# Optimization experiments

Hardware: AMD Instinct MI355X
Metric: run time of the kernel (lower is better)

## Reference

```python
import jax, jax.numpy as jnp
import numpy as np

SPARSITY = 0.01  # sparsity_threshold (softshrink lambda)


def _cas(n):
    # Hartley cas kernel: cos + sin
    t = jnp.arange(n, dtype=jnp.float32)
    a = 2.0 * jnp.pi * jnp.outer(t, t) / n
    return jnp.cos(a) + jnp.sin(a)


def _dht2d(x):
    # Faithful to source 4-D branch: transforms the LAST TWO axes (W and C)
    B, H, W, C = x.shape
    y = jnp.einsum('bhwc,cd->bhwd', x, _cas(C))          # contract channel axis
    return jnp.einsum('vw,bhwd->bhvd', _cas(W), y)       # contract width axis


def setup_inputs() -> dict:
    key = jax.random.key(0)
    k0, k1, k2, k3, k4 = jax.random.split(key, 5)
    B, H, W, C = 1, 180, 360, 512
    nb, bs, f = 8, 64, 1  # num_blocks, block_size, hidden_size_factor
    scale = 0.02
    x = jax.random.normal(k0, (B, H, W, C), jnp.float32)
    w1 = scale * jax.random.normal(k1, (2, nb, bs, bs * f), jnp.float32)
    b1 = scale * jax.random.normal(k2, (2, nb, bs * f), jnp.float32)
    w2 = scale * jax.random.normal(k3, (2, nb, bs * f, bs), jnp.float32)
    b2 = scale * jax.random.normal(k4, (2, nb, bs), jnp.float32)
    return {"x": x, "w1": w1, "b1": b1, "w2": w2, "b2": b2}


def reference(x, w1, b1, w2, b2):
    bias = x
    B, H, W, C = x.shape
    nb, bs = w1.shape[1], w1.shape[2]

    xh = _dht2d(x).reshape(B, H, W, nb, bs)                       # X_H_k
    xn = jnp.roll(jnp.flip(xh, axis=(1, 2)), shift=(1, 1), axis=(1, 2))  # X_H_{-k}

    # layer 1: 0.5*(Xk(w0+w1) + Xn(w0-w1)) + b  (algebraic regroup of the 4 einsums)
    w1a, w1b = w1[0] + w1[1], w1[0] - w1[1]
    o1k = jax.nn.relu(0.5 * (jnp.einsum('bhwki,kio->bhwko', xh, w1a)
                             + jnp.einsum('bhwki,kio->bhwko', xn, w1b)) + b1[0])
    o1n = jax.nn.relu(0.5 * (jnp.einsum('bhwki,kio->bhwko', xn, w1a)
                             + jnp.einsum('bhwki,kio->bhwko', xh, w1b)) + b1[1])

    # layer 2 (faithfully reproduces source bug: o2n consumes o2k, bias included)
    w2a, w2b = w2[0] + w2[1], w2[0] - w2[1]
    o2k = 0.5 * (jnp.einsum('bhwki,kio->bhwko', o1k, w2a)
                 + jnp.einsum('bhwki,kio->bhwko', o1n, w2b)) + b2[0]
    o2n = 0.5 * (jnp.einsum('bhwki,kio->bhwko', o1n, w2a)
                 + jnp.einsum('bhwki,kio->bhwko', o2k, w2b)) + b2[1]

    y = (o2k + o2n).reshape(B, H, W, C)
    y = jnp.sign(y) * jax.nn.relu(jnp.abs(y) - SPARSITY)          # softshrink
    y = _dht2d(y) / (W * C)                                       # idht2d normalization
    return y + bias
```

## Files before the change

kernel.cpp:

```cpp
#include <hip/hip_runtime.h>
#include <math.h>

#define HH 180
#define WDIM 360
#define CDIM 512
#define NP 64800
#define PL 184320

typedef unsigned short u16;
typedef __attribute__((ext_vector_type(8))) short short8;
typedef __attribute__((ext_vector_type(4))) float f4;

__device__ __forceinline__ u16 f2bf(float f){
    unsigned u = __float_as_uint(f);
    return (u16)((u + 0x7fffu + ((u >> 16) & 1u)) >> 16);
}
__device__ __forceinline__ void gl_lds16(const void* g, void* l){
    __builtin_amdgcn_global_load_lds((const __attribute__((address_space(1))) void*)g,
                                     (__attribute__((address_space(3))) void*)l, 16, 0, 0);
}

__global__ void prep(const float* __restrict__ w1, const float* __restrict__ w2,
                     u16* __restrict__ casC, u16* __restrict__ casW, u16* __restrict__ wts)
{
    int idx = blockIdx.x * 256 + threadIdx.x;
    if (idx < 512*512){
        int i = idx >> 9, j = idx & 511;
        int m = (i * j) & 511;
        float a = (float)m * (6.283185307179586f / 512.0f);
        float s, c; __sincosf(a, &s, &c);
        casC[idx] = f2bf(c + s);
    }
    if (idx < 360*384){
        int i = idx / 384, j = idx - (idx / 384) * 384;
        u16 v = 0;
        if (j < 360){
            int m = (i * j) % 360;
            float a = (float)m * (6.283185307179586f / 360.0f);
            float s, c; __sincosf(a, &s, &c);
            v = f2bf(c + s);
        }
        casW[idx] = v;
    }
    if (idx < 131072){
        int s = idx >> 15, r = idx & 32767;
        int kb = r >> 12, o = (r >> 6) & 63, ii = r & 63;
        const float* w = (s < 2) ? w1 : w2;
        float v0 = w[kb*4096 + ii*64 + o];
        float v1 = w[32768 + kb*4096 + ii*64 + o];
        float v = 0.5f * ((s & 1) ? (v0 - v1) : (v0 + v1));
        wts[idx] = f2bf(v);
    }
}

template<int ASTAGE, int STORE, int SWAP>
__global__ __launch_bounds__(256)
void gemm_k(const void* __restrict__ A, int ldA, long long sA, int clampA,
            const u16* __restrict__ B, int ldB, long long sB,
            void* __restrict__ C, long long sC, int Mreal,
            const float* __restrict__ X, float scale, int nK, int nbx)
{
    __shared__ u16 As[2][4096];
    __shared__ u16 Bs[2][4096];

    const int tid = threadIdx.x, wv = tid >> 6, l = tid & 63;
    const int l16 = l & 15, quad = l >> 4;
    const int z = blockIdx.z;

    int bx, by;
    if constexpr (SWAP){
        int n = gridDim.x;
        int q = n >> 3, r = n & 7;
        int xcd = blockIdx.x & 7, idx = blockIdx.x >> 3;
        int swz = (xcd < r ? xcd*(q+1) : r*(q+1) + (xcd-r)*q) + idx;
        bx = swz / nbx;
        by = swz - bx * nbx;
    } else {
        bx = blockIdx.x;
        by = blockIdx.y;
    }
    const int row0 = bx * 128, col0 = by * 128;

    const int rh = wv & 1, c0 = wv >> 1;

    const u16* gB = B + sB * z + (long long)(col0 + rh*64 + l) * ldB;

    const u16* gA = nullptr;
    const float* gAf = nullptr; int arow = 0, cb = 0;
    if constexpr (ASTAGE == 0){
        int r = row0 + rh*64 + l; r = r <= clampA ? r : clampA;
        gA = (const u16*)A + sA * z + (long long)r * ldA;
    } else {
        int r = row0 + (tid >> 1); r = r <= clampA ? r : clampA;
        gAf  = (const float*)A + (long long)r * ldA + (tid & 1) * 16;
        arow = tid >> 1;
        cb   = (tid & 1) * 2;
    }

    f4 acc[4][4];
    #pragma unroll
    for (int mt = 0; mt < 4; ++mt)
        #pragma unroll
        for (int nt = 0; nt < 4; ++nt)
            acc[mt][nt] = (f4)0.0f;

    const int mrow = (wv >> 1) * 64, ncol = (wv & 1) * 64;

    float4 f0, f1, f2, f3;

    auto stageB = [&](int buf, int k0){
        gl_lds16(gB + k0 + c0*8,     &Bs[buf][c0*1024     + rh*512]);
        gl_lds16(gB + k0 + (c0+2)*8, &Bs[buf][(c0+2)*1024 + rh*512]);
    };
    auto stageA = [&](int buf, int k0){
        gl_lds16(gA + k0 + c0*8,     &As[buf][c0*1024     + rh*512]);
        gl_lds16(gA + k0 + (c0+2)*8, &As[buf][(c0+2)*1024 + rh*512]);
    };
    auto issueA = [&](int k0){
        const float* p = gAf + k0;
        f0 = *(const float4*)(p);
        f1 = *(const float4*)(p + 4);
        f2 = *(const float4*)(p + 8);
        f3 = *(const float4*)(p + 12);
    };
    auto writeA = [&](int buf){
        uint4 w0, w1;
        w0.x = (unsigned)f2bf(f0.x) | ((unsigned)f2bf(f0.y) << 16);
        w0.y = (unsigned)f2bf(f0.z) | ((unsigned)f2bf(f0.w) << 16);
        w0.z = (unsigned)f2bf(f1.x) | ((unsigned)f2bf(f1.y) << 16);
        w0.w = (unsigned)f2bf(f1.z) | ((unsigned)f2bf(f1.w) << 16);
        w1.x = (unsigned)f2bf(f2.x) | ((unsigned)f2bf(f2.y) << 16);
        w1.y = (unsigned)f2bf(f2.z) | ((unsigned)f2bf(f2.w) << 16);
        w1.z = (unsigned)f2bf(f3.x) | ((unsigned)f2bf(f3.y) << 16);
        w1.w = (unsigned)f2bf(f3.z) | ((unsigned)f2bf(f3.w) << 16);
        *(uint4*)&As[buf][cb*1024     + arow*8] = w0;
        *(uint4*)&As[buf][(cb+1)*1024 + arow*8] = w1;
    };

    stageB(0, 0);
    if constexpr (ASTAGE == 0){
        stageA(0, 0);
    } else {
        issueA(0);
        writeA(0);
    }
    __syncthreads();

    int cur = 0;
    for (int kt = 0; kt < nK; ++kt){
        const bool more = (kt + 1 < nK);
        const int k0n = (kt + 1) * 32;
        if (more){
            stageB(cur ^ 1, k0n);
            if constexpr (ASTAGE == 0) stageA(cur ^ 1, k0n);
            else                       issueA(k0n);
        }
        short8 af[4];
        #pragma unroll
        for (int mt = 0; mt < 4; ++mt)
            af[mt] = *(const short8*)&As[cur][quad*1024 + (mrow + mt*16 + l16)*8];
        #pragma unroll
        for (int nt = 0; nt < 4; ++nt){
            short8 bfv = *(const short8*)&Bs[cur][quad*1024 + (ncol + nt*16 + l16)*8];
            #pragma unroll
            for (int mt = 0; mt < 4; ++mt)
                acc[mt][nt] = __builtin_amdgcn_mfma_f32_16x16x32_bf16(af[mt], bfv, acc[mt][nt], 0, 0, 0);
        }
        if constexpr (ASTAGE == 1){
            if (more) writeA(cur ^ 1);
        }
        __syncthreads();
        cur ^= 1;
    }

    #pragma unroll
    for (int mt = 0; mt < 4; ++mt){
        #pragma unroll
        for (int i = 0; i < 4; ++i){
            int gr = row0 + mrow + mt*16 + quad*4 + i;
            if (gr >= Mreal) continue;
            int th = 0, tw = 0;
            if constexpr (STORE == 1){ th = gr / 360; tw = gr - th * 360; }
            #pragma unroll
            for (int nt = 0; nt < 4; ++nt){
                int gc = col0 + ncol + nt*16 + l16;
                if constexpr (STORE == 0){
                    ((u16*)C)[sC*z + (long long)gr*512 + gc] = f2bf(acc[mt][nt][i]);
                } else if constexpr (STORE == 1){
                    ((u16*)C)[((long long)th*512 + gc)*360 + tw] = f2bf(acc[mt][nt][i]);
                } else {
                    long long off = sC*z + (long long)gr*512 + gc;
                    ((float*)C)[off] = fmaf(acc[mt][nt][i], scale, X[off]);
                }
            }
        }
    }
}

__global__ __launch_bounds__(256)
void mlp_k(const u16* __restrict__ xh, const u16* __restrict__ wts,
           const float* __restrict__ b1, const float* __restrict__ b2,
           u16* __restrict__ yout)
{
    __shared__ u16 sW0[64*72], sW1[64*72];
    __shared__ u16 sXh[64*72], sXn[64*72], s1k[64*72], s1n[64*72];
    __shared__ float sb[256];

    const int tid = threadIdx.x;
    const int wv = tid >> 6, l = tid & 63, lane16 = l & 15, quad = l >> 4;
    const int kb = blockIdx.y;
    const int p0 = blockIdx.x * 64;
    const int w16 = wv * 16;

    if (tid < 64){
        sb[tid]       = b1[kb*64 + tid];
        sb[64 + tid]  = b1[512 + kb*64 + tid];
        sb[128 + tid] = b2[kb*64 + tid];
        sb[192 + tid] = b2[512 + kb*64 + tid];
    }
    {
        const int r = tid >> 2, sg = (tid & 3) * 16;
        const u16* s0 = wts + kb*4096 + r*64 + sg;
        const u16* s1 = wts + 32768 + kb*4096 + r*64 + sg;
        *(uint4*)&sW0[r*72 + sg]     = *(const uint4*)s0;
        *(uint4*)&sW0[r*72 + sg + 8] = *(const uint4*)(s0 + 8);
        *(uint4*)&sW1[r*72 + sg]     = *(const uint4*)s1;
        *(uint4*)&sW1[r*72 + sg + 8] = *(const uint4*)(s1 + 8);

        int p = p0 + r; int pc = p <= 64799 ? p : 64799;
        int h = pc / 360; int v = pc - h * 360;
        int hn = (h == 0) ? 0 : (180 - h);
        int vn = (v == 0) ? 0 : (360 - v);
        long long bh = (long long)pc * 512 + kb*64 + sg;
        long long bn = (long long)(hn*360 + vn) * 512 + kb*64 + sg;
        *(uint4*)&sXh[r*72 + sg]     = *(const uint4*)&xh[bh];
        *(uint4*)&sXh[r*72 + sg + 8] = *(const uint4*)&xh[bh + 8];
        *(uint4*)&sXn[r*72 + sg]     = *(const uint4*)&xh[bn];
        *(uint4*)&sXn[r*72 + sg + 8] = *(const uint4*)&xh[bn + 8];
    }
    __syncthreads();

    f4 aK[4], aN[4];
    #pragma unroll
    for (int nt = 0; nt < 4; ++nt){ aK[nt] = (f4)0.0f; aN[nt] = (f4)0.0f; }
    #pragma unroll
    for (int kq = 0; kq < 2; ++kq){
        short8 fxh = *(const short8*)&sXh[(w16 + lane16)*72 + kq*32 + quad*8];
        short8 fxn = *(const short8*)&sXn[(w16 + lane16)*72 + kq*32 + quad*8];
        #pragma unroll
        for (int nt = 0; nt < 4; ++nt){
            short8 wa = *(const short8*)&sW0[(nt*16 + lane16)*72 + kq*32 + quad*8];
            short8 wb = *(const short8*)&sW1[(nt*16 + lane16)*72 + kq*32 + quad*8];
            aK[nt] = __builtin_amdgcn_mfma_f32_16x16x32_bf16(fxh, wa, aK[nt], 0,0,0);
            aK[nt] = __builtin_amdgcn_mfma_f32_16x16x32_bf16(fxn, wb, aK[nt], 0,0,0);
            aN[nt] = __builtin_amdgcn_mfma_f32_16x16x32_bf16(fxn, wa, aN[nt], 0,0,0);
            aN[nt] = __builtin_amdgcn_mfma_f32_16x16x32_bf16(fxh, wb, aN[nt], 0,0,0);
        }
    }
    #pragma unroll
    for (int nt = 0; nt < 4; ++nt){
        int cc = nt*16 + lane16;
        #pragma unroll
        for (int i = 0; i < 4; ++i){
            int rr = w16 + quad*4 + i;
            float vk = fmaxf(aK[nt][i] + sb[cc], 0.f);
            float vn = fmaxf(aN[nt][i] + sb[64 + cc], 0.f);
            s1k[rr*72 + cc] = f2bf(vk);
            s1n[rr*72 + cc] = f2bf(vn);
        }
    }
    __syncthreads();

    {
        const int r = tid >> 2, sg = (tid & 3) * 16;
        const u16* s0 = wts + 65536 + kb*4096 + r*64 + sg;
        const u16* s1 = wts + 98304 + kb*4096 + r*64 + sg;
        *(uint4*)&sW0[r*72 + sg]     = *(const uint4*)s0;
        *(uint4*)&sW0[r*72 + sg + 8] = *(const uint4*)(s0 + 8);
        *(uint4*)&sW1[r*72 + sg]     = *(const uint4*)s1;
        *(uint4*)&sW1[r*72 + sg + 8] = *(const uint4*)(s1 + 8);
    }
    __syncthreads();

    f4 k2[4];
    #pragma unroll
    for (int nt = 0; nt < 4; ++nt) k2[nt] = (f4)0.0f;
    #pragma unroll
    for (int kq = 0; kq < 2; ++kq){
        short8 a1k = *(const short8*)&s1k[(w16 + lane16)*72 + kq*32 + quad*8];
        short8 a1n = *(const short8*)&s1n[(w16 + lane16)*72 + kq*32 + quad*8];
        #pragma unroll
        for (int nt = 0; nt < 4; ++nt){
            short8 wa = *(const short8*)&sW0[(nt*16 + lane16)*72 + kq*32 + quad*8];
            short8 wb = *(const short8*)&sW1[(nt*16 + lane16)*72 + kq*32 + quad*8];
            k2[nt] = __builtin_amdgcn_mfma_f32_16x16x32_bf16(a1k, wa, k2[nt], 0,0,0);
            k2[nt] = __builtin_amdgcn_mfma_f32_16x16x32_bf16(a1n, wb, k2[nt], 0,0,0);
        }
    }
    #pragma unroll
    for (int nt = 0; nt < 4; ++nt){
        int cc = nt*16 + lane16;
        #pragma unroll
        for (int i = 0; i < 4; ++i){
            int rr = w16 + quad*4 + i;
            float v2 = k2[nt][i] + sb[128 + cc];
            k2[nt][i] = v2;
            sXh[rr*72 + cc] = f2bf(v2);
        }
    }
    __syncthreads();

    f4 n2[4];
    #pragma unroll
    for (int nt = 0; nt < 4; ++nt) n2[nt] = (f4)0.0f;
    #pragma unroll
    for (int kq = 0; kq < 2; ++kq){
        short8 a1n = *(const short8*)&s1n[(w16 + lane16)*72 + kq*32 + quad*8];
        short8 a2k = *(const short8*)&sXh[(w16 + lane16)*72 + kq*32 + quad*8];
        #pragma unroll
        for (int nt = 0; nt < 4; ++nt){
            short8 wa = *(const short8*)&sW0[(nt*16 + lane16)*72 + kq*32 + quad*8];
            short8 wb = *(const short8*)&sW1[(nt*16 + lane16)*72 + kq*32 + quad*8];
            n2[nt] = __builtin_amdgcn_mfma_f32_16x16x32_bf16(a1n, wa, n2[nt], 0,0,0);
            n2[nt] = __builtin_amdgcn_mfma_f32_16x16x32_bf16(a2k, wb, n2[nt], 0,0,0);
        }
    }
    #pragma unroll
    for (int nt = 0; nt < 4; ++nt){
        int cc = nt*16 + lane16;
        #pragma unroll
        for (int i = 0; i < 4; ++i){
            int rr = w16 + quad*4 + i;
            int p = p0 + rr;
            float y = k2[nt][i] + n2[nt][i] + sb[192 + cc];
            float ay = fabsf(y) - 0.01f;
            float r0 = ay > 0.f ? (y > 0.f ? ay : -ay) : 0.f;
            if (p < 64800) yout[(long long)p * 512 + kb*64 + cc] = f2bf(r0);
        }
    }
}

extern "C" void kernel_launch(void* const* d_in, const int* in_sizes, int n_in,
                              void* d_out, int out_size, void* d_ws, size_t ws_size,
                              hipStream_t stream) {
    const float* x  = (const float*)d_in[0];
    const float* w1 = (const float*)d_in[1];
    const float* b1 = (const float*)d_in[2];
    const float* w2 = (const float*)d_in[3];
    const float* b2 = (const float*)d_in[4];
    float* out = (float*)d_out;

    u16* ws   = (u16*)d_ws;
    u16* casC = ws;
    u16* casW = casC + 262144;
    u16* wts  = casW + 138240;
    u16* bufT = wts  + 131072;
    u16* bufP = bufT + 33177664;

    prep<<<1024, 256, 0, stream>>>(w1, w2, casC, casW, wts);

    dim3 gBig(2028, 1, 1);
    dim3 gW(3, 4, 180);
    dim3 gM(1013, 8, 1);

    gemm_k<1,1,1><<<gBig, 256, 0, stream>>>(x, 512, 0, 64799,
                                            casC, 512, 0,
                                            bufT, 0, 64800, nullptr, 0.f, 16, 4);
    gemm_k<0,0,0><<<gW, 256, 0, stream>>>(casW, 384, 0, 359,
                                          bufT, 360, (long long)PL,
                                          bufP, (long long)PL, 360, nullptr, 0.f, 12, 1);
    mlp_k<<<gM, 256, 0, stream>>>(bufP, wts, b1, b2, bufT);
    gemm_k<0,1,1><<<gBig, 256, 0, stream>>>(bufT, 512, 0, 64799,
                                            casC, 512, 0,
                                            bufP, 0, 64800, nullptr, 0.f, 16, 4);
    gemm_k<0,2,0><<<gW, 256, 0, stream>>>(casW, 384, 0, 359,
                                          bufP, 360, (long long)PL,
                                          out, (long long)PL, 360,
                                          x, 1.0f/184320.0f, 12, 1);
}
```

Measured before the change: 706.8 us.

## Pre-convert input to bf16 and use triple-buffered async LDS pipeline in GEMM

Adds a separate conversion kernel that turns the fp32 input into bf16, so every GEMM can stage A through direct global-to-LDS loads instead of register loads plus conversion. The GEMM main loop moves from double buffering to a three-stage ring: prefetch runs three tiles ahead, with explicit vmcnt waits and raw barriers in place of __syncthreads. This aims to hide global latency better and remove conversion work from the inner loop. The cost is an extra kernel pass over the input, 50% more LDS per block, and redundant clamped reloads of the last tile near the end of the loop.

```diff
diff --git a/kernel.cpp b/kernel.cpp
--- a/kernel.cpp
+++ b/kernel.cpp
@@ -53,15 +53,29 @@
     }
 }
 
-template<int ASTAGE, int STORE, int SWAP>
 __global__ __launch_bounds__(256)
-void gemm_k(const void* __restrict__ A, int ldA, long long sA, int clampA,
+void cvt_k(const float* __restrict__ x, u16* __restrict__ xb)
+{
+    long long i = ((long long)blockIdx.x * 256 + threadIdx.x) * 8;
+    float4 a = *(const float4*)(x + i);
+    float4 b = *(const float4*)(x + i + 4);
+    uint4 w;
+    w.x = (unsigned)f2bf(a.x) | ((unsigned)f2bf(a.y) << 16);
+    w.y = (unsigned)f2bf(a.z) | ((unsigned)f2bf(a.w) << 16);
+    w.z = (unsigned)f2bf(b.x) | ((unsigned)f2bf(b.y) << 16);
+    w.w = (unsigned)f2bf(b.z) | ((unsigned)f2bf(b.w) << 16);
+    *(uint4*)(xb + i) = w;
+}
+
+template<int STORE, int SWAP>
+__global__ __launch_bounds__(256)
+void gemm_k(const u16* __restrict__ A, int ldA, long long sA, int clampA,
             const u16* __restrict__ B, int ldB, long long sB,
             void* __restrict__ C, long long sC, int Mreal,
             const float* __restrict__ X, float scale, int nK, int nbx)
 {
-    __shared__ u16 As[2][4096];
-    __shared__ u16 Bs[2][4096];
+    __shared__ u16 As[3][4096];
+    __shared__ u16 Bs[3][4096];
 
     const int tid = threadIdx.x, wv = tid >> 6, l = tid & 63;
     const int l16 = l & 15, quad = l >> 4;
@@ -84,18 +98,8 @@
     const int rh = wv & 1, c0 = wv >> 1;
 
     const u16* gB = B + sB * z + (long long)(col0 + rh*64 + l) * ldB;
-
-    const u16* gA = nullptr;
-    const float* gAf = nullptr; int arow = 0, cb = 0;
-    if constexpr (ASTAGE == 0){
-        int r = row0 + rh*64 + l; r = r <= clampA ? r : clampA;
-        gA = (const u16*)A + sA * z + (long long)r * ldA;
-    } else {
-        int r = row0 + (tid >> 1); r = r <= clampA ? r : clampA;
-        gAf  = (const float*)A + (long long)r * ldA + (tid & 1) * 16;
-        arow = tid >> 1;
-        cb   = (tid & 1) * 2;
-    }
+    int ar = row0 + rh*64 + l; ar = ar <= clampA ? ar : clampA;
+    const u16* gA = A + sA * z + (long long)ar * ldA;
 
     f4 acc[4][4];
     #pragma unroll
@@ -106,55 +110,22 @@
 
     const int mrow = (wv >> 1) * 64, ncol = (wv & 1) * 64;
 
-    float4 f0, f1, f2, f3;
-
-    auto stageB = [&](int buf, int k0){
-        gl_lds16(gB + k0 + c0*8,     &Bs[buf][c0*1024     + rh*512]);
-        gl_lds16(gB + k0 + (c0+2)*8, &Bs[buf][(c0+2)*1024 + rh*512]);
-    };
-    auto stageA = [&](int buf, int k0){
-        gl_lds16(gA + k0 + c0*8,     &As[buf][c0*1024     + rh*512]);
-        gl_lds16(gA + k0 + (c0+2)*8, &As[buf][(c0+2)*1024 + rh*512]);
-    };
-    auto issueA = [&](int k0){
-        const float* p = gAf + k0;
-        f0 = *(const float4*)(p);
-        f1 = *(const float4*)(p + 4);
-        f2 = *(const float4*)(p + 8);
-        f3 = *(const float4*)(p + 12);
-    };
-    auto writeA = [&](int buf){
-        uint4 w0, w1;
-        w0.x = (unsigned)f2bf(f0.x) | ((unsigned)f2bf(f0.y) << 16);
-        w0.y = (unsigned)f2bf(f0.z) | ((unsigned)f2bf(f0.w) << 16);
-        w0.z = (unsigned)f2bf(f1.x) | ((unsigned)f2bf(f1.y) << 16);
-        w0.w = (unsigned)f2bf(f1.z) | ((unsigned)f2bf(f1.w) << 16);
-        w1.x = (unsigned)f2bf(f2.x) | ((unsigned)f2bf(f2.y) << 16);
-        w1.y = (unsigned)f2bf(f2.z) | ((unsigned)f2bf(f2.w) << 16);
-        w1.z = (unsigned)f2bf(f3.x) | ((unsigned)f2bf(f3.y) << 16);
-        w1.w = (unsigned)f2bf(f3.z) | ((unsigned)f2bf(f3.w) << 16);
-        *(uint4*)&As[buf][cb*1024     + arow*8] = w0;
-        *(uint4*)&As[buf][(cb+1)*1024 + arow*8] = w1;
-    };
-
-    stageB(0, 0);
-    if constexpr (ASTAGE == 0){
-        stageA(0, 0);
-    } else {
-        issueA(0);
-        writeA(0);
-    }
-    __syncthreads();
+    #define STAGE(buf, kt) do{ const int k0_ = (kt)*32;                          \
+        gl_lds16(gB + k0_ + c0*8,     &Bs[buf][c0*1024     + rh*512]);           \
+        gl_lds16(gB + k0_ + (c0+2)*8, &Bs[buf][(c0+2)*1024 + rh*512]);           \
+        gl_lds16(gA + k0_ + c0*8,     &As[buf][c0*1024     + rh*512]);           \
+        gl_lds16(gA + k0_ + (c0+2)*8, &As[buf][(c0+2)*1024 + rh*512]); }while(0)
+
+    STAGE(0, 0);
+    STAGE(1, 1);
+    STAGE(2, 2);
 
     int cur = 0;
     for (int kt = 0; kt < nK; ++kt){
-        const bool more = (kt + 1 < nK);
-        const int k0n = (kt + 1) * 32;
-        if (more){
-            stageB(cur ^ 1, k0n);
-            if constexpr (ASTAGE == 0) stageA(cur ^ 1, k0n);
-            else                       issueA(k0n);
-        }
+        asm volatile("s_waitcnt vmcnt(8)" ::: "memory");
+        __builtin_amdgcn_s_barrier();
+        __builtin_amdgcn_sched_barrier(0);
+
         short8 af[4];
         #pragma unroll
         for (int mt = 0; mt < 4; ++mt)
@@ -166,12 +137,16 @@
             for (int mt = 0; mt < 4; ++mt)
                 acc[mt][nt] = __builtin_amdgcn_mfma_f32_16x16x32_bf16(af[mt], bfv, acc[mt][nt], 0, 0, 0);
         }
-        if constexpr (ASTAGE == 1){
-            if (more) writeA(cur ^ 1);
-        }
-        __syncthreads();
-        cur ^= 1;
-    }
+
+        __builtin_amdgcn_sched_barrier(0);
+        __builtin_amdgcn_s_barrier();
+        __builtin_amdgcn_sched_barrier(0);
+
+        int nxt = kt + 3; if (nxt > nK - 1) nxt = nK - 1;
+        STAGE(cur, nxt);
+        cur = (cur == 2) ? 0 : cur + 1;
+    }
+    #undef STAGE
 
     #pragma unroll
     for (int mt = 0; mt < 4; ++mt){
@@ -358,23 +333,24 @@
     u16* bufP = bufT + 33177664;
 
     prep<<<1024, 256, 0, stream>>>(w1, w2, casC, casW, wts);
+    cvt_k<<<16200, 256, 0, stream>>>(x, bufP);
 
     dim3 gBig(2028, 1, 1);
     dim3 gW(3, 4, 180);
     dim3 gM(1013, 8, 1);
 
-    gemm_k<1,1,1><<<gBig, 256, 0, stream>>>(x, 512, 0, 64799,
-                                            casC, 512, 0,
-                                            bufT, 0, 64800, nullptr, 0.f, 16, 4);
-    gemm_k<0,0,0><<<gW, 256, 0, stream>>>(casW, 384, 0, 359,
-                                          bufT, 360, (long long)PL,
-                                          bufP, (long long)PL, 360, nullptr, 0.f, 12, 1);
+    gemm_k<1,1><<<gBig, 256, 0, stream>>>(bufP, 512, 0, 64799,
+                                          casC, 512, 0,
+                                          bufT, 0, 64800, nullptr, 0.f, 16, 4);
+    gemm_k<0,0><<<gW, 256, 0, stream>>>(casW, 384, 0, 359,
+                                        bufT, 360, (long long)PL,
+                                        bufP, (long long)PL, 360, nullptr, 0.f, 12, 1);
     mlp_k<<<gM, 256, 0, stream>>>(bufP, wts, b1, b2, bufT);
-    gemm_k<0,1,1><<<gBig, 256, 0, stream>>>(bufT, 512, 0, 64799,
-                                            casC, 512, 0,
-                                            bufP, 0, 64800, nullptr, 0.f, 16, 4);
-    gemm_k<0,2,0><<<gW, 256, 0, stream>>>(casW, 384, 0, 359,
-                                          bufP, 360, (long long)PL,
-                                          out, (long long)PL, 360,
-                                          x, 1.0f/184320.0f, 12, 1);
-}
+    gemm_k<1,1><<<gBig, 256, 0, stream>>>(bufT, 512, 0, 64799,
+                                          casC, 512, 0,
+                                          bufP, 0, 64800, nullptr, 0.f, 16, 4);
+    gemm_k<2,0><<<gW, 256, 0, stream>>>(casW, 384, 0, 359,
+                                        bufP, 360, (long long)PL,
+                                        out, (long long)PL, 360,
+                                        x, 1.0f/184320.0f, 12, 1);
+}
```

Result: slower. 772.2 us (+9.3%).
